# Kernel optimization log

Measured on AMD Instinct MI355X. Metric: run time of the kernel, lower is better.

Reference implementation:

```python
import jax, jax.numpy as jnp
import numpy as np

B, S, I, H = 2, 400, 80, 128
F = 2 * H            # bidirectional feature dim
N = S + 1            # zero row prepended -> pairwise grid size
MAX_SEG = 50
NCLS = 50


def prelu(x, a):
    return jnp.where(x >= 0, x, a * x)


def lstm_dir(x, Wi, Wh, b, reverse=False):
    # x: (B, S, I); torch gate order: i, f, g, o
    if reverse:
        x = x[:, ::-1]
    Hd = Wh.shape[1]

    def step(carry, xt):
        h, c = carry
        gates = xt @ Wi.T + h @ Wh.T + b
        i_, f_, g_, o_ = jnp.split(gates, 4, axis=-1)
        c = jax.nn.sigmoid(f_) * c + jax.nn.sigmoid(i_) * jnp.tanh(g_)
        h = jax.nn.sigmoid(o_) * jnp.tanh(c)
        return (h, c), h

    h0 = jnp.zeros((x.shape[0], Hd), x.dtype)
    _, hs = jax.lax.scan(step, (h0, h0), jnp.swapaxes(x, 0, 1))
    hs = jnp.swapaxes(hs, 0, 1)
    if reverse:
        hs = hs[:, ::-1]
    return hs


def setup_inputs() -> dict:
    key = jax.random.key(0)
    ks = jax.random.split(key, 16)

    def rn(k, shape, s=0.05):
        return jax.random.normal(k, shape, jnp.float32) * s

    inp = {
        "x": jax.random.normal(ks[0], (B, S, I), jnp.float32),
        "lengths": jnp.full((B,), S, jnp.int32),
        "Wi_f": rn(ks[1], (4 * H, I)), "Wh_f": rn(ks[2], (4 * H, H)), "b_f": jnp.zeros((4 * H,), jnp.float32),
        "Wi_b": rn(ks[3], (4 * H, I)), "Wh_b": rn(ks[4], (4 * H, H)), "b_b": jnp.zeros((4 * H,), jnp.float32),
        "a1": jnp.full((1,), 0.25, jnp.float32),
        "W1": rn(ks[5], (100, 3 * F)), "b1": jnp.zeros((100,), jnp.float32),
        "a2": jnp.full((1,), 0.25, jnp.float32),
        "W2": rn(ks[6], (1, 100)), "b2": jnp.zeros((1,), jnp.float32),
        "ac1": jnp.full((1,), 0.25, jnp.float32),
        "Wc1": rn(ks[7], (2 * NCLS, F)), "bc1": jnp.zeros((2 * NCLS,), jnp.float32),
        "ac2": jnp.full((1,), 0.25, jnp.float32),
        "Wc2": rn(ks[8], (NCLS, 2 * NCLS)), "bc2": jnp.zeros((NCLS,), jnp.float32),
        "ab1": jnp.full((1,), 0.25, jnp.float32),
        "Wb1": rn(ks[9], (2 * NCLS, F)), "bb1": jnp.zeros((2 * NCLS,), jnp.float32),
        "ab2": jnp.full((1,), 0.25, jnp.float32),
        "Wb2": rn(ks[10], (2, 2 * NCLS)), "bb2": jnp.zeros((2,), jnp.float32),
    }
    return inp


def compute_scores(x, Wi_f, Wh_f, b_f, Wi_b, Wh_b, b_b, a1, W1, b1, a2, W2, b2):
    rnn_out = jnp.concatenate(
        [lstm_dir(x, Wi_f, Wh_f, b_f, False), lstm_dir(x, Wi_b, Wh_b, b_b, True)], axis=-1
    )  # (B, S, F)
    xp = jnp.concatenate([jnp.zeros((x.shape[0], 1, F), x.dtype), rnn_out], axis=1)  # (B, N, F)
    cum = jnp.cumsum(xp, axis=1)
    # phi[b,i,j] = concat(cum[j]-cum[i], xp[i], xp[j]); PReLU is elementwise with a
    # single shared parameter, and the first Linear is additive across the concat
    # blocks, so we decompose W1 instead of materializing the (B,N,N,3F) tensor.
    W1c, W1d, W1e = W1[:, :F], W1[:, F:2 * F], W1[:, 2 * F:]
    pc = prelu(cum[:, None, :, :] - cum[:, :, None, :], a1)  # (B, N, N, F)
    pxd = prelu(xp, a1) @ W1d.T                              # (B, N, 100)
    pxe = prelu(xp, a1) @ W1e.T                              # (B, N, 100)
    h = jnp.einsum('bijf,kf->bijk', pc, W1c) + pxd[:, :, None, :] + pxe[:, None, :, :] + b1
    scores = (prelu(h, a2) @ W2.T + b2)[..., 0]              # (B, N, N)
    return rnn_out, scores


def segment_search(scores):
    # DP: best[i] = max_{max(0,i-MAX_SEG) <= k < i} best[k] + scores[:, k, i]
    Bn, Nn = scores.shape[0], scores.shape[1]
    ks = jnp.arange(Nn)

    def dp_step(best, i):
        col = jnp.take(scores, i, axis=2)                    # (B, N)
        mask = (ks >= i - MAX_SEG) & (ks < i)
        cand = jnp.where(mask[None, :], best + col, -jnp.inf)
        m = cand.max(axis=1)
        k = cand.argmax(axis=1)
        best = best.at[:, i].set(m)
        return best, k

    best0 = jnp.zeros((Bn, Nn), scores.dtype)
    best, prev_tail = jax.lax.scan(dp_step, best0, jnp.arange(1, Nn))
    prev = jnp.concatenate([jnp.zeros((Bn, 1), jnp.int32),
                            prev_tail.T.astype(jnp.int32)], axis=1)  # (B, N)
    return best, prev


def reference(x, lengths, Wi_f, Wh_f, b_f, Wi_b, Wh_b, b_b, a1, W1, b1, a2, W2, b2,
              ac1, Wc1, bc1, ac2, Wc2, bc2, ab1, Wb1, bb1, ab2, Wb2, bb2):
    rnn_out, scores = compute_scores(x, Wi_f, Wh_f, b_f, Wi_b, Wh_b, b_b,
                                     a1, W1, b1, a2, W2, b2)
    cls_out = prelu(prelu(rnn_out, ac1) @ Wc1.T + bc1, ac2) @ Wc2.T + bc2
    bin_out = prelu(prelu(rnn_out, ab1) @ Wb1.T + bb1, ab2) @ Wb2.T + bb2
    best, prev = segment_search(scores)
    # pred score for the best segmentation ending at `lengths[b]` equals best[b, L]
    pred_scores = best[jnp.arange(scores.shape[0]), lengths]
    return scores, cls_out, bin_out, pred_scores, prev
```

## Files before the change

kernel.cpp:

```cpp
#include <hip/hip_runtime.h>
#include <hip/hip_fp16.h>
#include <math.h>

#define BB 2
#define SS 400
#define II 80
#define HH 128
#define FF 256
#define NN 401
#define G4 512
#define MAXSEG 50
#define NCLS 50
#define KH 100
#define KP 112
#define FRAGF 14336

#define SCORES_OFF 0
#define CLS_OFF    (BB*NN*NN)
#define BIN_OFF    (CLS_OFF + BB*SS*NCLS)
#define PRED_OFF   (BIN_OFF + BB*SS*2)
#define PREV_OFF   (PRED_OFF + BB)

#define WS_GX      0
#define WS_RNN     (WS_GX + 4*SS*G4)
#define WS_CUM     (WS_RNN + BB*SS*FF)
#define WS_PXD     (WS_CUM + BB*NN*FF)
#define WS_PXE     (WS_PXD + BB*NN*KP)
#define WS_PART    (WS_PXE + BB*NN*KP)
#define WS_W2P     (WS_PART + BB*16*FF)
#define WS_B1P     (WS_W2P + KP)
#define WS_WHP     (WS_B1P + KP)
#define WS_WFRAGC  (WS_WHP + 65536)
#define WS_WFRAGD  (WS_WFRAGC + FRAGF)
#define WS_WFRAGE  (WS_WFRAGD + FRAGF)
#define WS_WFRAGHC (WS_WFRAGE + FRAGF)
#define WS_WFRAGHB (WS_WFRAGHC + FRAGF)
#define WS_BC1P    (WS_WFRAGHB + FRAGF)
#define WS_BB1P    (WS_BC1P + KP)

typedef __attribute__((ext_vector_type(8))) short short8;
typedef __attribute__((ext_vector_type(4))) float f32x4;
typedef _Float16 f16x2 __attribute__((ext_vector_type(2)));
typedef _Float16 f16x8 __attribute__((ext_vector_type(8)));

__device__ __forceinline__ float prelu_f(float x, float a) {
    return x >= 0.f ? x : a * x;
}
__device__ __forceinline__ unsigned short f2bf(float x) {
    union { float f; unsigned u; } v; v.f = x;
    unsigned r = v.u + 0x7fffu + ((v.u >> 16) & 1u);
    return (unsigned short)(r >> 16);
}
__device__ __forceinline__ unsigned cvt_pk_bf16(float lo, float hi) {
    unsigned r;
    asm("v_cvt_pk_bf16_f32 %0, %1, %2" : "=v"(r) : "v"(lo), "v"(hi));
    return r;
}
__device__ __forceinline__ float fast_sigmoid(float x) {
    return 1.f / (1.f + __expf(-x));
}
__device__ __forceinline__ float fast_tanh(float x) {
    return 1.f - 2.f / (1.f + __expf(2.f * x));
}
__device__ __forceinline__ void rec_barrier() {
    __builtin_amdgcn_sched_barrier(0);
    asm volatile("s_waitcnt lgkmcnt(0)");
    __builtin_amdgcn_s_barrier();
    __builtin_amdgcn_sched_barrier(0);
}
__device__ __forceinline__ int fragidx(int k, int f) {
    int kt = k >> 4, l15 = k & 15;
    int ks = f >> 5, quad = (f >> 3) & 3, e = f & 7;
    return ((((kt * 8 + ks) * 4 + quad) * 16) + l15) * 8 + e;
}

#define GXTC 8
#define GXBLKS (4 * (SS / GXTC))
#define PREPBLKS (G4 + GXBLKS)
__global__ void k_lstm_pre(const float* __restrict__ x,
                           const float* __restrict__ Wi_f, const float* __restrict__ b_f,
                           const float* __restrict__ Wi_b, const float* __restrict__ b_b,
                           float* __restrict__ gx,
                           const float* __restrict__ Wh_f, const float* __restrict__ Wh_b,
                           __half* __restrict__ whp) {
    int blk0 = blockIdx.x;
    int tid = threadIdx.x;
    if (blk0 < G4) {
        int gq = blk0;
        int gate = gq >> 7;
        int unit = gq & 127;
        int wv = unit >> 4, col = unit & 15;
        int dir = tid >> 7, k = tid & 127;
        int kt = k >> 5, lanehi = (k >> 3) & 3, e = k & 7;
        int lane = lanehi * 16 + col;
        const float* Wh = dir ? Wh_b : Wh_f;
        whp[(size_t)(((((dir * 4 + gate) * 8 + wv) * 4 + kt) * 64) + lane) * 8 + e] =
            (__half)Wh[gq * HH + k];
        return;
    }
    int gxb = blk0 - G4;
    int db = gxb / (SS / GXTC);
    int tc = gxb % (SS / GXTC);
    int b = db & 1, dir = db >> 1;
    const float* Wi = dir ? Wi_b : Wi_f;
    const float* bias = dir ? b_b : b_f;
    int t0 = tc * GXTC;

    __shared__ __align__(16) float xs[GXTC][II];
    for (int idx = tid; idx < GXTC * II; idx += 256) {
        int tt = idx / II, ii = idx - tt * II;
        int xt = dir ? (SS - 1 - (t0 + tt)) : (t0 + tt);
        xs[tt][ii] = x[(b * SS + xt) * II + ii];
    }
    __syncthreads();

    int g1 = tid + 256;
    const float* w0p = Wi + tid * II;
    const float* w1p = Wi + g1 * II;
    float acc0[GXTC], acc1[GXTC];
    {
        float b0v = bias[tid], b1v = bias[g1];
#pragma unroll
        for (int t = 0; t < GXTC; ++t) { acc0[t] = b0v; acc1[t] = b1v; }
    }
    for (int kc = 0; kc < 5; ++kc) {
        float4 wa0 = *(const float4*)(w0p + kc * 16 + 0);
        float4 wa1 = *(const float4*)(w0p + kc * 16 + 4);
        float4 wa2 = *(const float4*)(w0p + kc * 16 + 8);
        float4 wa3 = *(const float4*)(w0p + kc * 16 + 12);
        float4 wb0 = *(const float4*)(w1p + kc * 16 + 0);
        float4 wb1 = *(const float4*)(w1p + kc * 16 + 4);
        float4 wb2 = *(const float4*)(w1p + kc * 16 + 8);
        float4 wb3 = *(const float4*)(w1p + kc * 16 + 12);
#pragma unroll
        for (int t = 0; t < GXTC; ++t) {
            float4 x0 = *(const float4*)(&xs[t][kc * 16 + 0]);
            float4 x1 = *(const float4*)(&xs[t][kc * 16 + 4]);
            float4 x2 = *(const float4*)(&xs[t][kc * 16 + 8]);
            float4 x3 = *(const float4*)(&xs[t][kc * 16 + 12]);
            acc0[t] += wa0.x * x0.x + wa0.y * x0.y + wa0.z * x0.z + wa0.w * x0.w;
            acc0[t] += wa1.x * x1.x + wa1.y * x1.y + wa1.z * x1.z + wa1.w * x1.w;
            acc0[t] += wa2.x * x2.x + wa2.y * x2.y + wa2.z * x2.z + wa2.w * x2.w;
            acc0[t] += wa3.x * x3.x + wa3.y * x3.y + wa3.z * x3.z + wa3.w * x3.w;
            acc1[t] += wb0.x * x0.x + wb0.y * x0.y + wb0.z * x0.z + wb0.w * x0.w;
            acc1[t] += wb1.x * x1.x + wb1.y * x1.y + wb1.z * x1.z + wb1.w * x1.w;
            acc1[t] += wb2.x * x2.x + wb2.y * x2.y + wb2.z * x2.z + wb2.w * x2.w;
            acc1[t] += wb3.x * x3.x + wb3.y * x3.y + wb3.z * x3.z + wb3.w * x3.w;
        }
    }
#pragma unroll
    for (int t = 0; t < GXTC; ++t) {
        gx[((size_t)(db * SS + t0 + t) * HH + (tid & 127)) * 4 + (tid >> 7)] = acc0[t];
        gx[((size_t)(db * SS + t0 + t) * HH + (g1 & 127)) * 4 + (g1 >> 7)] = acc1[t];
    }
}

#define WPACKS (5 * KP)
__global__ __launch_bounds__(256, 1)
void k_lstm_rec(const _Float16* __restrict__ whf, const float* __restrict__ gxr,
                float* __restrict__ rnn_out,
                const float* __restrict__ W1, const float* __restrict__ W2,
                const float* __restrict__ b1,
                const float* __restrict__ Wc1, const float* __restrict__ Wb1,
                const float* __restrict__ bc1, const float* __restrict__ bb1,
                short* __restrict__ wfC, short* __restrict__ wfD,
                short* __restrict__ wfE, short* __restrict__ wfHC,
                short* __restrict__ wfHB,
                float* __restrict__ w2p, float* __restrict__ b1p,
                float* __restrict__ bc1p, float* __restrict__ bb1p) {
    int tid = threadIdx.x;
    if (blockIdx.x >= 4) {
        int blk0 = blockIdx.x - 4;
        int which = blk0 / KP;
        int k = blk0 % KP;
        float w = 0.f;
        short* dst = wfC;
        if (which == 0)      { if (k < KH) w = W1[k * (3 * FF) + tid];          dst = wfC; }
        else if (which == 1) { if (k < KH) w = W1[k * (3 * FF) + FF + tid];     dst = wfD; }
        else if (which == 2) { if (k < KH) w = W1[k * (3 * FF) + 2 * FF + tid]; dst = wfE; }
        else if (which == 3) { if (k < KH) w = Wc1[k * FF + tid];               dst = wfHC; }
        else                 { if (k < KH) w = Wb1[k * FF + tid];               dst = wfHB; }
        dst[fragidx(k, tid)] = (short)f2bf(w);
        if (tid == 0) {
            if (which == 0) {
                w2p[k] = (k < KH) ? W2[k] : 0.f;
                b1p[k] = (k < KH) ? b1[k] : 0.f;
            } else if (which == 3) {
                bc1p[k] = (k < KH) ? bc1[k] : 0.f;
            } else if (which == 4) {
                bb1p[k] = (k < KH) ? bb1[k] : 0.f;
            }
        }
        return;
    }
    int db = blockIdx.x;
    int b = db & 1, dir = db >> 1;
    int wv = tid >> 6;
    int lane = tid & 63;

    f16x8 bfA[4][4], bfB[4][4];
    {
        const f16x8* wp = (const f16x8*)whf;
#pragma unroll
        for (int g = 0; g < 4; ++g)
#pragma unroll
            for (int kt = 0; kt < 4; ++kt) {
                bfA[g][kt] = wp[((((dir * 4 + g) * 8 + (2 * wv)) * 4 + kt) * 64) + lane];
                bfB[g][kt] = wp[((((dir * 4 + g) * 8 + (2 * wv + 1)) * 4 + kt) * 64) + lane];
            }
    }

    __shared__ __align__(16) __half hsf[2][128];
    (&hsf[0][0])[tid] = (__half)0.f;
    __syncthreads();

    bool act = (lane < 32);
    bool grpB = (lane >= 16);
    int unit = (wv << 5) + (lane & 31);
    float c_state = 0.f;

    const float4* gp4 = (const float4*)gxr + (size_t)(db * SS) * HH + unit;
    float4 g0 = make_float4(0,0,0,0), g1 = g0, g2 = g0, g3 = g0;
    if (act) {
        g0 = gp4[0 * HH];
        g1 = gp4[1 * HH];
        g2 = gp4[2 * HH];
        g3 = gp4[3 * HH];
    }
    const float4* gq = gp4 + (size_t)4 * HH;

    float* outp = rnn_out + ((size_t)b * SS + (dir ? (SS - 1) : 0)) * FF
                + dir * HH + unit;
    const int ostep = dir ? -FF : FF;

    const f32x4 z4 = (f32x4){0.f, 0.f, 0.f, 0.f};
    int pb = 0;
    int hib = (lane >> 4) * 8;
    bool aload = (lane & 3) == 0;

    f16x8 a0v = (f16x8)(_Float16)0.f, a1v = a0v, a2v = a0v, a3v = a0v;

#define REC_STEP(G, PF) do {                                                   \
        if (aload) {                                                           \
            a0v = *(const f16x8*)(&hsf[pb][ 0 + hib]);                         \
            a1v = *(const f16x8*)(&hsf[pb][32 + hib]);                         \
            a2v = *(const f16x8*)(&hsf[pb][64 + hib]);                         \
            a3v = *(const f16x8*)(&hsf[pb][96 + hib]);                         \
        }                                                                      \
        f32x4 aA0 = __builtin_amdgcn_mfma_f32_16x16x32_f16(a0v, bfA[0][0], z4, 0, 0, 0); \
        f32x4 aA1 = __builtin_amdgcn_mfma_f32_16x16x32_f16(a0v, bfA[1][0], z4, 0, 0, 0); \
        f32x4 aA2 = __builtin_amdgcn_mfma_f32_16x16x32_f16(a0v, bfA[2][0], z4, 0, 0, 0); \
        f32x4 aA3 = __builtin_amdgcn_mfma_f32_16x16x32_f16(a0v, bfA[3][0], z4, 0, 0, 0); \
        f32x4 aB0 = __builtin_amdgcn_mfma_f32_16x16x32_f16(a0v, bfB[0][0], z4, 0, 0, 0); \
        f32x4 aB1 = __builtin_amdgcn_mfma_f32_16x16x32_f16(a0v, bfB[1][0], z4, 0, 0, 0); \
        f32x4 aB2 = __builtin_amdgcn_mfma_f32_16x16x32_f16(a0v, bfB[2][0], z4, 0, 0, 0); \
        f32x4 aB3 = __builtin_amdgcn_mfma_f32_16x16x32_f16(a0v, bfB[3][0], z4, 0, 0, 0); \
        aA0 = __builtin_amdgcn_mfma_f32_16x16x32_f16(a1v, bfA[0][1], aA0, 0, 0, 0); \
        aA1 = __builtin_amdgcn_mfma_f32_16x16x32_f16(a1v, bfA[1][1], aA1, 0, 0, 0); \
        aA2 = __builtin_amdgcn_mfma_f32_16x16x32_f16(a1v, bfA[2][1], aA2, 0, 0, 0); \
        aA3 = __builtin_amdgcn_mfma_f32_16x16x32_f16(a1v, bfA[3][1], aA3, 0, 0, 0); \
        aB0 = __builtin_amdgcn_mfma_f32_16x16x32_f16(a1v, bfB[0][1], aB0, 0, 0, 0); \
        aB1 = __builtin_amdgcn_mfma_f32_16x16x32_f16(a1v, bfB[1][1], aB1, 0, 0, 0); \
        aB2 = __builtin_amdgcn_mfma_f32_16x16x32_f16(a1v, bfB[2][1], aB2, 0, 0, 0); \
        aB3 = __builtin_amdgcn_mfma_f32_16x16x32_f16(a1v, bfB[3][1], aB3, 0, 0, 0); \
        aA0 = __builtin_amdgcn_mfma_f32_16x16x32_f16(a2v, bfA[0][2], aA0, 0, 0, 0); \
        aA1 = __builtin_amdgcn_mfma_f32_16x16x32_f16(a2v, bfA[1][2], aA1, 0, 0, 0); \
        aA2 = __builtin_amdgcn_mfma_f32_16x16x32_f16(a2v, bfA[2][2], aA2, 0, 0, 0); \
        aA3 = __builtin_amdgcn_mfma_f32_16x16x32_f16(a2v, bfA[3][2], aA3, 0, 0, 0); \
        aB0 = __builtin_amdgcn_mfma_f32_16x16x32_f16(a2v, bfB[0][2], aB0, 0, 0, 0); \
        aB1 = __builtin_amdgcn_mfma_f32_16x16x32_f16(a2v, bfB[1][2], aB1, 0, 0, 0); \
        aB2 = __builtin_amdgcn_mfma_f32_16x16x32_f16(a2v, bfB[2][2], aB2, 0, 0, 0); \
        aB3 = __builtin_amdgcn_mfma_f32_16x16x32_f16(a2v, bfB[3][2], aB3, 0, 0, 0); \
        aA0 = __builtin_amdgcn_mfma_f32_16x16x32_f16(a3v, bfA[0][3], aA0, 0, 0, 0); \
        aA1 = __builtin_amdgcn_mfma_f32_16x16x32_f16(a3v, bfA[1][3], aA1, 0, 0, 0); \
        aA2 = __builtin_amdgcn_mfma_f32_16x16x32_f16(a3v, bfA[2][3], aA2, 0, 0, 0); \
        aA3 = __builtin_amdgcn_mfma_f32_16x16x32_f16(a3v, bfA[3][3], aA3, 0, 0, 0); \
        aB0 = __builtin_amdgcn_mfma_f32_16x16x32_f16(a3v, bfB[0][3], aB0, 0, 0, 0); \
        aB1 = __builtin_amdgcn_mfma_f32_16x16x32_f16(a3v, bfB[1][3], aB1, 0, 0, 0); \
        aB2 = __builtin_amdgcn_mfma_f32_16x16x32_f16(a3v, bfB[2][3], aB2, 0, 0, 0); \
        aB3 = __builtin_amdgcn_mfma_f32_16x16x32_f16(a3v, bfB[3][3], aB3, 0, 0, 0); \
        if (act) {                                                             \
            float gi = (grpB ? aB0[0] : aA0[0]) + G.x;                         \
            float gf = (grpB ? aB1[0] : aA1[0]) + G.y;                         \
            float gg = (grpB ? aB2[0] : aA2[0]) + G.z;                         \
            float go = (grpB ? aB3[0] : aA3[0]) + G.w;                         \
            if (PF) { G = *gq; gq += HH; }         \
            c_state = fast_sigmoid(gf) * c_state + fast_sigmoid(gi) * fast_tanh(gg); \
            float h = fast_sigmoid(go) * fast_tanh(c_state);                   \
            hsf[pb ^ 1][unit] = (__half)h;                                     \
            *outp = h;                                                         \
            outp += ostep;                                                     \
        }                                                                      \
        rec_barrier();                                                         \
        pb ^= 1;                                                               \
    } while (0)

    for (int it = 0; it < 99; ++it) {
        REC_STEP(g0, 1);
        REC_STEP(g1, 1);
        REC_STEP(g2, 1);
        REC_STEP(g3, 1);
    }
    REC_STEP(g0, 0);
    REC_STEP(g1, 0);
    REC_STEP(g2, 0);
    REC_STEP(g3, 0);
#undef REC_STEP
}

#define PXBLKS 26
#define HDBLKS 25
#define AP 272
#define UCP 116
__global__ __launch_bounds__(256, 2)
void k_cum_mlp(const float* __restrict__ rnn, float* __restrict__ cum,
               const float* __restrict__ a1p,
               const float* __restrict__ ac1p, const float* __restrict__ ab1p,
               const short* __restrict__ wfD, const short* __restrict__ wfE,
               const short* __restrict__ wfHC, const short* __restrict__ wfHB,
               const float* __restrict__ bc1p, const float* __restrict__ bb1p,
               const float* __restrict__ ac2p, const float* __restrict__ ab2p,
               const float* __restrict__ Wc2, const float* __restrict__ bc2,
               const float* __restrict__ Wb2, const float* __restrict__ bb2,
               float* __restrict__ pxd, float* __restrict__ pxe,
               float* __restrict__ cls_out, float* __restrict__ bin_out) {
    int tid = threadIdx.x;
    if (blockIdx.x < BB) {
        int b = blockIdx.x;
        int f = tid;
        float run = 0.f;
        cum[(size_t)(b * NN) * FF + f] = 0.f;
        const float* rp = rnn + (size_t)b * SS * FF + f;
        float* cp = cum + ((size_t)b * NN + 1) * FF + f;
#pragma unroll 8
        for (int t = 0; t < SS; ++t) {
            run += rp[(size_t)t * FF];
            cp[(size_t)t * FF] = run;
        }
        return;
    }
    int blk = blockIdx.x - BB;
    bool is_px = (blk < PXBLKS);
    int rowbase = is_px ? blk * 32 : (blk - PXBLKS) * 32;
    int nrows_tot = is_px ? BB * NN : BB * SS;

    __shared__ __align__(16) short dth[2][32][AP];
    __shared__ float ucsh[2][32][UCP];

    {
        int row = tid >> 3;
        int fb = (tid & 7) * 32;
        int rg = rowbase + row;
        float src[32];
        if (is_px) {
            float a1 = a1p[0];
            int b = rg / NN, n = rg % NN;
            bool valid = (rg < nrows_tot) && (n > 0);
            const float* sp = valid ? (rnn + (b * SS + n - 1) * FF + fb) : nullptr;
#pragma unroll
            for (int c4 = 0; c4 < 8; ++c4) {
                float4 v = valid ? *(const float4*)(sp + c4 * 4) : make_float4(0,0,0,0);
                src[c4*4] = v.x; src[c4*4+1] = v.y; src[c4*4+2] = v.z; src[c4*4+3] = v.w;
            }
            union { short8 s; unsigned u4[4]; } h8;
#pragma unroll
            for (int c8 = 0; c8 < 4; ++c8) {
                float d[8];
#pragma unroll
                for (int e = 0; e < 8; ++e) d[e] = prelu_f(src[c8*8+e], a1);
#pragma unroll
                for (int p = 0; p < 4; ++p) h8.u4[p] = cvt_pk_bf16(d[2*p], d[2*p+1]);
                *(short8*)(&dth[0][row][fb + c8 * 8]) = h8.s;
            }
        } else {
            float ac1 = ac1p[0], ab1 = ab1p[0];
            bool valid = (rg < nrows_tot);
            const float* sp = valid ? (rnn + rg * FF + fb) : nullptr;
#pragma unroll
            for (int c4 = 0; c4 < 8; ++c4) {
                float4 v = valid ? *(const float4*)(sp + c4 * 4) : make_float4(0,0,0,0);
                src[c4*4] = v.x; src[c4*4+1] = v.y; src[c4*4+2] = v.z; src[c4*4+3] = v.w;
            }
            union { short8 s; unsigned u4[4]; } hc, hb;
#pragma unroll
            for (int c8 = 0; c8 < 4; ++c8) {
                float dc[8], dbv[8];
#pragma unroll
                for (int e = 0; e < 8; ++e) {
                    dc[e] = prelu_f(src[c8*8+e], ac1);
                    dbv[e] = prelu_f(src[c8*8+e], ab1);
                }
#pragma unroll
                for (int p = 0; p < 4; ++p) {
                    hc.u4[p] = cvt_pk_bf16(dc[2*p], dc[2*p+1]);
                    hb.u4[p] = cvt_pk_bf16(dbv[2*p], dbv[2*p+1]);
                }
                *(short8*)(&dth[0][row][fb + c8 * 8]) = hc.s;
                *(short8*)(&dth[1][row][fb + c8 * 8]) = hb.s;
            }
        }
    }
    __syncthreads();

    int lane = tid & 63;
    int wv = tid >> 6;
    int quad = lane >> 4;
    int l15 = lane & 15;
    int kt0 = wv * 2, kt1 = wv * 2 + 1;
    bool has1 = (kt1 < 7);

    const short8* wp0 = (const short8*)(is_px ? wfD : wfHC);
    const short8* wp1 = (const short8*)(is_px ? wfE : wfHB);

    f32x4 acc[2][2][2];
#pragma unroll
    for (int p = 0; p < 2; ++p)
#pragma unroll
        for (int mt = 0; mt < 2; ++mt)
#pragma unroll
            for (int kk = 0; kk < 2; ++kk) acc[p][mt][kk] = (f32x4){0.f,0.f,0.f,0.f};

#pragma unroll
    for (int ks = 0; ks < 8; ++ks) {
        short8 b00 = wp0[((kt0 * 8 + ks) * 4 + quad) * 16 + l15];
        short8 b01 = has1 ? wp0[((kt1 * 8 + ks) * 4 + quad) * 16 + l15] : b00;
        short8 b10 = wp1[((kt0 * 8 + ks) * 4 + quad) * 16 + l15];
        short8 b11 = has1 ? wp1[((kt1 * 8 + ks) * 4 + quad) * 16 + l15] : b10;
#pragma unroll
        for (int mt = 0; mt < 2; ++mt) {
            short8 a0 = *(const short8*)(&dth[0][mt * 16 + l15][ks * 32 + quad * 8]);
            short8 a1v = is_px ? a0
                       : *(const short8*)(&dth[1][mt * 16 + l15][ks * 32 + quad * 8]);
            acc[0][mt][0] = __builtin_amdgcn_mfma_f32_16x16x32_bf16(a0, b00, acc[0][mt][0], 0, 0, 0);
            acc[1][mt][0] = __builtin_amdgcn_mfma_f32_16x16x32_bf16(a1v, b10, acc[1][mt][0], 0, 0, 0);
            if (has1) {
                acc[0][mt][1] = __builtin_amdgcn_mfma_f32_16x16x32_bf16(a0, b01, acc[0][mt][1], 0, 0, 0);
                acc[1][mt][1] = __builtin_amdgcn_mfma_f32_16x16x32_bf16(a1v, b11, acc[1][mt][1], 0, 0, 0);
            }
        }
    }

    int kout0 = kt0 * 16 + l15;
    int kout1 = has1 ? (kt1 * 16 + l15) : 0;

    if (is_px) {
#pragma unroll
        for (int mt = 0; mt < 2; ++mt) {
#pragma unroll
            for (int r = 0; r < 4; ++r) {
                int m = mt * 16 + quad * 4 + r;
                int rg = rowbase + m;
                if (rg < nrows_tot) {
                    pxd[rg * KP + kout0] = acc[0][mt][0][r];
                    pxe[rg * KP + kout0] = acc[1][mt][0][r];
                    if (has1) {
                        pxd[rg * KP + kout1] = acc[0][mt][1][r];
                        pxe[rg * KP + kout1] = acc[1][mt][1][r];
                    }
                }
            }
        }
        return;
    }

    float bc0 = bc1p[kout0], bc1v = bc1p[kout1];
    float bb0 = bb1p[kout0], bb1v = bb1p[kout1];
    float ac2 = ac2p[0], ab2 = ab2p[0];
#pragma unroll
    for (int mt = 0; mt < 2; ++mt) {
#pragma unroll
        for (int r = 0; r < 4; ++r) {
            int m = mt * 16 + quad * 4 + r;
            ucsh[0][m][kout0] = prelu_f(acc[0][mt][0][r] + bc0, ac2);
            ucsh[1][m][kout0] = prelu_f(acc[1][mt][0][r] + bb0, ab2);
            if (has1) {
                ucsh[0][m][kout1] = prelu_f(acc[0][mt][1][r] + bc1v, ac2);
                ucsh[1][m][kout1] = prelu_f(acc[1][mt][1][r] + bb1v, ab2);
            }
        }
    }
    __syncthreads();
    {
        int row = tid >> 3;
        int oc = tid & 7;
        int rg = rowbase + row;
        bool valid = (rg < nrows_tot);
        for (int o = oc; o < NCLS; o += 8) {
            float s = bc2[o];
            const float* w = Wc2 + o * KH;
#pragma unroll 4
            for (int k = 0; k < KH; ++k) s += w[k] * ucsh[0][row][k];
            if (valid) cls_out[rg * NCLS + o] = s;
        }
        if (tid < 64) {
            int row2 = tid >> 1, o = tid & 1;
            int rg2 = rowbase + row2;
            float s = bb2[o];
            const float* w = Wb2 + o * KH;
#pragma unroll 4
            for (int k = 0; k < KH; ++k) s += w[k] * ucsh[1][row2][k];
            if (rg2 < nrows_tot) bin_out[rg2 * 2 + o] = s;
        }
    }
}

#define JT 32
#define JTILES 13
#define NP2 201
#define APS 280
#define CIP 264
__global__ __launch_bounds__(256, 3)
void k_scores(const float* __restrict__ cum,
              const short* __restrict__ wfrag,
              const float* __restrict__ pxd, const float* __restrict__ pxe,
              const float* __restrict__ b1p, const float* __restrict__ w2p,
              const float* __restrict__ b2p,
              const float* __restrict__ a1p, const float* __restrict__ a2p,
              float* __restrict__ scores, float* __restrict__ dpcol) {
    int blk = blockIdx.x;
    int jt = blk % JTILES;
    int ipair = (blk / JTILES) % NP2;
    int b = blk / (JTILES * NP2);
    int tid = threadIdx.x;
    float a1 = a1p[0], a2 = a2p[0];
    int jbase = jt * JT;
    int i0 = ipair * 2;
    int i1 = i0 + 1;
    bool has_i1 = (i1 <= SS);
    int i1c = has_i1 ? i1 : i0;

    __shared__ __align__(16) float cish[2][CIP];
    __shared__ __align__(16) short dth[2][JT][APS];
    __shared__ float red[2][4][JT];

    cish[0][tid + (tid >> 5)] = cum[(b * NN + i0) * FF + tid];
    cish[1][tid + (tid >> 5)] = cum[(b * NN + i1c) * FF + tid];
    __syncthreads();

    {
        int row = tid >> 3;
        int fb = (tid & 7) * 32;
        int fbq = fb + (tid & 7);
        int jg = jbase + row;
        int jc = (jg <= SS) ? jg : SS;
        const float* cj = cum + (b * NN + jc) * FF + fb;
        float4 v[8];
#pragma unroll
        for (int c8 = 0; c8 < 4; ++c8) {
            v[2 * c8] = *(const float4*)(cj + c8 * 8);
            v[2 * c8 + 1] = *(const float4*)(cj + c8 * 8 + 4);
        }
#pragma unroll
        for (int ii = 0; ii < 2; ++ii) {
            const float* cio = &cish[ii][0];
#pragma unroll
            for (int c8 = 0; c8 < 4; ++c8) {
                float dv[8] = { v[2*c8].x, v[2*c8].y, v[2*c8].z, v[2*c8].w,
                                v[2*c8+1].x, v[2*c8+1].y, v[2*c8+1].z, v[2*c8+1].w };
                float d[8];
#pragma unroll
                for (int e = 0; e < 8; ++e)
                    d[e] = prelu_f(dv[e] - cio[fbq + c8 * 8 + e], a1);
                union { short8 s; unsigned u4[4]; } h8;
#pragma unroll
                for (int p = 0; p < 4; ++p) h8.u4[p] = cvt_pk_bf16(d[2*p], d[2*p+1]);
                *(short8*)(&dth[ii][row][fb + c8 * 8]) = h8.s;
            }
        }
    }
    __syncthreads();

    int lane = tid & 63;
    int wv = tid >> 6;
    int quad = lane >> 4;
    int l15 = lane & 15;
    int kt0 = wv * 2, kt1 = wv * 2 + 1;
    bool has1 = (kt1 < 7);

    const short8* wf = (const short8*)wfrag;
    f32x4 acc[2][2][2];
#pragma unroll
    for (int ii = 0; ii < 2; ++ii)
#pragma unroll
        for (int mt = 0; mt < 2; ++mt)
#pragma unroll
            for (int kk = 0; kk < 2; ++kk) acc[ii][mt][kk] = (f32x4){0.f,0.f,0.f,0.f};

#pragma unroll
    for (int ks = 0; ks < 8; ++ks) {
        short8 b0 = wf[((kt0 * 8 + ks) * 4 + quad) * 16 + l15];
        short8 b1v = has1 ? wf[((kt1 * 8 + ks) * 4 + quad) * 16 + l15] : b0;
#pragma unroll
        for (int ii = 0; ii < 2; ++ii) {
#pragma unroll
            for (int mt = 0; mt < 2; ++mt) {
                short8 a = *(const short8*)(&dth[ii][mt * 16 + l15][ks * 32 + quad * 8]);
                acc[ii][mt][0] = __builtin_amdgcn_mfma_f32_16x16x32_bf16(a, b0, acc[ii][mt][0], 0, 0, 0);
                if (has1)
                    acc[ii][mt][1] = __builtin_amdgcn_mfma_f32_16x16x32_bf16(a, b1v, acc[ii][mt][1], 0, 0, 0);
            }
        }
    }

    int kout0 = kt0 * 16 + l15;
    int kout1 = has1 ? (kt1 * 16 + l15) : 0;
    float bb0 = b1p[kout0], bb1v = b1p[kout1];
    float w20 = w2p[kout0];
    float w21 = has1 ? w2p[kout1] : 0.f;

#pragma unroll
    for (int ii = 0; ii < 2; ++ii) {
        int iv = ii ? i1c : i0;
        float pd0 = pxd[(b * NN + iv) * KP + kout0];
        float pd1 = pxd[(b * NN + iv) * KP + kout1];
#pragma unroll
        for (int mt = 0; mt < 2; ++mt) {
#pragma unroll
            for (int r = 0; r < 4; ++r) {
                int m = mt * 16 + quad * 4 + r;
                int jg = jbase + m;
                int jc = (jg <= SS) ? jg : SS;
                float pe0 = pxe[(b * NN + jc) * KP + kout0];
                float pe1 = pxe[(b * NN + jc) * KP + kout1];
                float h0 = acc[ii][mt][0][r] + pd0 + pe0 + bb0;
                float s = w20 * prelu_f(h0, a2);
                float h1 = acc[ii][mt][1][r] + pd1 + pe1 + bb1v;
                s += w21 * prelu_f(h1, a2);
                s += __shfl_xor(s, 1);
                s += __shfl_xor(s, 2);
                s += __shfl_xor(s, 4);
                s += __shfl_xor(s, 8);
                if (l15 == 0) red[ii][wv][m] = s;
            }
        }
    }
    __syncthreads();
    if (tid < 2 * JT) {
        int ii = tid >> 5;
        int jl = tid & 31;
        int jg = jbase + jl;
        int iv = ii ? i1 : i0;
        if (jg <= SS && (ii == 0 || has_i1)) {
            float tot = red[ii][0][jl] + red[ii][1][jl] + red[ii][2][jl] + red[ii][3][jl] + b2p[0];
            scores[(b * NN + iv) * NN + jg] = tot;
            int d = jg - iv;
            if (d >= 1 && d <= MAXSEG) {
                dpcol[(b * NN + jg) * 64 + (iv & 63)] = tot;
            }
        }
    }
}

__global__ void k_dp(const float* __restrict__ dpcol, const int* __restrict__ lengths,
                     float* __restrict__ predF, float* __restrict__ prevF) {
    int b = blockIdx.x;
    int lane = threadIdx.x;
    int len = lengths[b];
    if (lane == 0) prevF[b * NN] = 0.f;

    float blr = 0.f;
    float predv = 0.f;

#define LO(I) (((I) > MAXSEG) ? ((I) - MAXSEG) : 0)
#define LOADCOL(ii) \
    ( ((ii) <= SS && (((lane - LO(ii)) & 63) < ((ii) - LO(ii)))) \
        ? dpcol[(b * NN + (ii)) * 64 + lane] : 0.f )

    float u0 = LOADCOL(1),  u1 = LOADCOL(2),  u2 = LOADCOL(3),  u3 = LOADCOL(4);
    float u4 = LOADCOL(5),  u5 = LOADCOL(6),  u6 = LOADCOL(7),  u7 = LOADCOL(8);
    float u8 = LOADCOL(9),  u9 = LOADCOL(10), u10 = LOADCOL(11), u11 = LOADCOL(12);
    float u12 = LOADCOL(13), u13 = LOADCOL(14), u14 = LOADCOL(15), u15 = LOADCOL(16);

#define DPP_MAX2(CTRL, va, vb) do {                                           \
        int _ta = __builtin_amdgcn_update_dpp(__float_as_int(va),             \
                      __float_as_int(va), (CTRL), 0xF, 0xF, false);           \
        int _tb = __builtin_amdgcn_update_dpp(__float_as_int(vb),             \
                      __float_as_int(vb), (CTRL), 0xF, 0xF, false);           \
        (va) = fmaxf((va), __int_as_float(_ta));                              \
        (vb) = fmaxf((vb), __int_as_float(_tb));                              \
    } while (0)

#define DP_STEP2(I, BUFA, BUFB) do {                                          \
        int loA_ = LO(I);                                                     \
        int cntA_ = (I) - loA_;                                               \
        int loB_ = LO((I) + 1);                                               \
        int cntBm_ = (I) - loB_;                   \
        int offA_ = (lane - loA_) & 63;                                       \
        int offB_ = (lane - loB_) & 63;                                       \
        float vA0_ = (offA_ < cntA_) ? blr + BUFA : -INFINITY;                \
        float vB0_ = (offB_ < cntBm_) ? blr + BUFB : -INFINITY;               \
        float vA_ = vA0_, vB_ = vB0_;                                         \
        DPP_MAX2(0x111, vA_, vB_);                            \
        DPP_MAX2(0x112, vA_, vB_);                            \
        DPP_MAX2(0x114, vA_, vB_);                            \
        DPP_MAX2(0x118, vA_, vB_);                            \
        DPP_MAX2(0x142, vA_, vB_);                          \
        DPP_MAX2(0x143, vA_, vB_);                          \
        float mA_ = __int_as_float(                                           \
            __builtin_amdgcn_readlane(__float_as_int(vA_), 63));              \
        float mB_ = __int_as_float(                                           \
            __builtin_amdgcn_readlane(__float_as_int(vB_), 63));              \
        float sI_ = __int_as_float(                                           \
            __builtin_amdgcn_readlane(__float_as_int(BUFB), (I) & 63));       \
        float candI_ = mA_ + sI_;                                             \
        bool takeI_ = candI_ > mB_;                                           \
        float mBf_ = takeI_ ? candI_ : mB_;                                   \
        unsigned long long mkA_ = __ballot(vA0_ == mA_);                      \
        unsigned long long mkB_ = __ballot(vB0_ == mB_);                      \
        int rotA_ = loA_ & 63;                                                \
        int rotB_ = loB_ & 63;                                                \
        unsigned long long mrA_ = rotA_ ? ((mkA_ >> rotA_) | (mkA_ << (64 - rotA_))) : mkA_; \
        unsigned long long mrB_ = rotB_ ? ((mkB_ >> rotB_) | (mkB_ << (64 - rotB_))) : mkB_; \
        int kbA_ = loA_ + (__ffsll(mrA_) - 1);                                \
        int kbB_ = takeI_ ? (I) : (loB_ + (__ffsll(mrB_) - 1));               \
        if (lane == 0) {                                                      \
            prevF[b * NN + (I)] = (float)kbA_;                                \
            prevF[b * NN + (I) + 1] = (float)kbB_;                            \
            if ((I) == len) predv = mA_;                                      \
            if ((I) + 1 == len) predv = mBf_;                                 \
        }                                                                     \
        if (lane == ((I) & 63)) blr = mA_;                                    \
        if (lane == (((I) + 1) & 63)) blr = mBf_;                             \
    } while (0)

    for (int i = 1; i <= SS; i += 16) {
        DP_STEP2(i,      u0,  u1);  u0 = LOADCOL(i + 16);  u1 = LOADCOL(i + 17);
        DP_STEP2(i + 2,  u2,  u3);  u2 = LOADCOL(i + 18);  u3 = LOADCOL(i + 19);
        DP_STEP2(i + 4,  u4,  u5);  u4 = LOADCOL(i + 20);  u5 = LOADCOL(i + 21);
        DP_STEP2(i + 6,  u6,  u7);  u6 = LOADCOL(i + 22);  u7 = LOADCOL(i + 23);
        DP_STEP2(i + 8,  u8,  u9);  u8 = LOADCOL(i + 24);  u9 = LOADCOL(i + 25);
        DP_STEP2(i + 10, u10, u11); u10 = LOADCOL(i + 26); u11 = LOADCOL(i + 27);
        DP_STEP2(i + 12, u12, u13); u12 = LOADCOL(i + 28); u13 = LOADCOL(i + 29);
        DP_STEP2(i + 14, u14, u15); u14 = LOADCOL(i + 30); u15 = LOADCOL(i + 31);
    }
#undef DP_STEP2
#undef DPP_MAX2
#undef LOADCOL
#undef LO
    if (lane == 0) predF[b] = predv;
}

extern "C" void kernel_launch(void* const* d_in, const int* in_sizes, int n_in,
                              void* d_out, int out_size, void* d_ws, size_t ws_size,
                              hipStream_t stream) {
    const float* x    = (const float*)d_in[0];
    const int* lengths= (const int*)d_in[1];
    const float* Wi_f = (const float*)d_in[2];
    const float* Wh_f = (const float*)d_in[3];
    const float* b_f  = (const float*)d_in[4];
    const float* Wi_b = (const float*)d_in[5];
    const float* Wh_b = (const float*)d_in[6];
    const float* b_b  = (const float*)d_in[7];
    const float* a1   = (const float*)d_in[8];
    const float* W1   = (const float*)d_in[9];
    const float* b1   = (const float*)d_in[10];
    const float* a2   = (const float*)d_in[11];
    const float* W2   = (const float*)d_in[12];
    const float* b2   = (const float*)d_in[13];
    const float* ac1  = (const float*)d_in[14];
    const float* Wc1  = (const float*)d_in[15];
    const float* bc1  = (const float*)d_in[16];
    const float* ac2  = (const float*)d_in[17];
    const float* Wc2  = (const float*)d_in[18];
    const float* bc2  = (const float*)d_in[19];
    const float* ab1  = (const float*)d_in[20];
    const float* Wb1  = (const float*)d_in[21];
    const float* bb1  = (const float*)d_in[22];
    const float* ab2  = (const float*)d_in[23];
    const float* Wb2  = (const float*)d_in[24];
    const float* bb2  = (const float*)d_in[25];

    float* out = (float*)d_out;
    float* scores = out + SCORES_OFF;
    float* cls    = out + CLS_OFF;
    float* bin    = out + BIN_OFF;
    float* pred   = out + PRED_OFF;
    float* prev   = out + PREV_OFF;

    float* ws    = (float*)d_ws;
    float* gx    = ws + WS_GX;
    float* dpcol = ws + WS_GX;
    float* rnn   = ws + WS_RNN;
    float* cum   = ws + WS_CUM;
    float* pxd   = ws + WS_PXD;
    float* pxe   = ws + WS_PXE;
    float* w2p   = ws + WS_W2P;
    float* b1p   = ws + WS_B1P;
    __half* whp  = (__half*)(ws + WS_WHP);
    short* wfC   = (short*)(ws + WS_WFRAGC);
    short* wfD   = (short*)(ws + WS_WFRAGD);
    short* wfE   = (short*)(ws + WS_WFRAGE);
    short* wfHC  = (short*)(ws + WS_WFRAGHC);
    short* wfHB  = (short*)(ws + WS_WFRAGHB);
    float* bc1p  = ws + WS_BC1P;
    float* bb1p  = ws + WS_BB1P;

    k_lstm_pre<<<PREPBLKS, 256, 0, stream>>>(x, Wi_f, b_f, Wi_b, b_b, gx,
                                             Wh_f, Wh_b, whp);
    k_lstm_rec<<<4 + WPACKS, 256, 0, stream>>>((const _Float16*)whp, gx, rnn,
                                               W1, W2, b1, Wc1, Wb1, bc1, bb1,
                                               wfC, wfD, wfE, wfHC, wfHB,
                                               w2p, b1p, bc1p, bb1p);
    k_cum_mlp<<<BB + PXBLKS + HDBLKS, 256, 0, stream>>>(rnn, cum, a1, ac1, ab1,
                                                        wfD, wfE, wfHC, wfHB,
                                                        bc1p, bb1p, ac2, ab2,
                                                        Wc2, bc2, Wb2, bb2,
                                                        pxd, pxe, cls, bin);
    k_scores<<<BB * NP2 * JTILES, 256, 0, stream>>>(cum, wfC, pxd, pxe, b1p, w2p, b2,
                                                    a1, a2, scores, dpcol);
    k_dp<<<BB, 64, 0, stream>>>(dpcol, lengths, pred, prev);
}
```

Baseline: 524.1 us.

## Merge both LSTM directions into one 512-thread block per batch

The recurrent LSTM kernel now runs both directions of a batch element in one 512-thread block, with 4 waves per direction and separate shared hidden-state buffers, instead of one 256-thread block per (batch, direction). The aim is to let waves from both directions share a CU's SIMDs and interleave their MFMA and activation work to hide per-step latency. In exchange, each step's barrier now waits on 8 waves across two independent recurrences, which couples their timing. The weight-packing blocks are also launched at 512 threads, with the upper half returning immediately.

New measurement: 624.6 us. 1.19x slower.

```diff
diff --git a/kernel.cpp b/kernel.cpp
--- a/kernel.cpp
+++ b/kernel.cpp
@@ -156,7 +156,7 @@
 }
 
 #define WPACKS (5 * KP)
-__global__ __launch_bounds__(256, 1)
+__global__ __launch_bounds__(512, 1)
 void k_lstm_rec(const _Float16* __restrict__ whf, const float* __restrict__ gxr,
                 float* __restrict__ rnn_out,
                 const float* __restrict__ W1, const float* __restrict__ W2,
@@ -169,8 +169,9 @@
                 float* __restrict__ w2p, float* __restrict__ b1p,
                 float* __restrict__ bc1p, float* __restrict__ bb1p) {
     int tid = threadIdx.x;
-    if (blockIdx.x >= 4) {
-        int blk0 = blockIdx.x - 4;
+    if (blockIdx.x >= BB) {
+        if (tid >= 256) return;
+        int blk0 = blockIdx.x - BB;
         int which = blk0 / KP;
         int k = blk0 % KP;
         float w = 0.f;
@@ -193,10 +194,12 @@
         }
         return;
     }
-    int db = blockIdx.x;
-    int b = db & 1, dir = db >> 1;
+    int b = blockIdx.x;
     int wv = tid >> 6;
+    int dir = wv >> 2;
+    int wvd = wv & 3;
     int lane = tid & 63;
+    int db = dir * 2 + b;
 
     f16x8 bfA[4][4], bfB[4][4];
     {
@@ -205,18 +208,18 @@
         for (int g = 0; g < 4; ++g)
 #pragma unroll
             for (int kt = 0; kt < 4; ++kt) {
-                bfA[g][kt] = wp[((((dir * 4 + g) * 8 + (2 * wv)) * 4 + kt) * 64) + lane];
-                bfB[g][kt] = wp[((((dir * 4 + g) * 8 + (2 * wv + 1)) * 4 + kt) * 64) + lane];
-            }
-    }
-
-    __shared__ __align__(16) __half hsf[2][128];
-    (&hsf[0][0])[tid] = (__half)0.f;
+                bfA[g][kt] = wp[((((dir * 4 + g) * 8 + (2 * wvd)) * 4 + kt) * 64) + lane];
+                bfB[g][kt] = wp[((((dir * 4 + g) * 8 + (2 * wvd + 1)) * 4 + kt) * 64) + lane];
+            }
+    }
+
+    __shared__ __align__(16) __half hsf[2][2][128];
+    (&hsf[0][0][0])[tid] = (__half)0.f;
     __syncthreads();
 
     bool act = (lane < 32);
     bool grpB = (lane >= 16);
-    int unit = (wv << 5) + (lane & 31);
+    int unit = (wvd << 5) + (lane & 31);
     float c_state = 0.f;
 
     const float4* gp4 = (const float4*)gxr + (size_t)(db * SS) * HH + unit;
@@ -242,10 +245,10 @@
 
 #define REC_STEP(G, PF) do {                                                   \
         if (aload) {                                                           \
-            a0v = *(const f16x8*)(&hsf[pb][ 0 + hib]);                         \
-            a1v = *(const f16x8*)(&hsf[pb][32 + hib]);                         \
-            a2v = *(const f16x8*)(&hsf[pb][64 + hib]);                         \
-            a3v = *(const f16x8*)(&hsf[pb][96 + hib]);                         \
+            a0v = *(const f16x8*)(&hsf[dir][pb][ 0 + hib]);                    \
+            a1v = *(const f16x8*)(&hsf[dir][pb][32 + hib]);                    \
+            a2v = *(const f16x8*)(&hsf[dir][pb][64 + hib]);                    \
+            a3v = *(const f16x8*)(&hsf[dir][pb][96 + hib]);                    \
         }                                                                      \
         f32x4 aA0 = __builtin_amdgcn_mfma_f32_16x16x32_f16(a0v, bfA[0][0], z4, 0, 0, 0); \
         f32x4 aA1 = __builtin_amdgcn_mfma_f32_16x16x32_f16(a0v, bfA[1][0], z4, 0, 0, 0); \
@@ -287,7 +290,7 @@
             if (PF) { G = *gq; gq += HH; }         \
             c_state = fast_sigmoid(gf) * c_state + fast_sigmoid(gi) * fast_tanh(gg); \
             float h = fast_sigmoid(go) * fast_tanh(c_state);                   \
-            hsf[pb ^ 1][unit] = (__half)h;                                     \
+            hsf[dir][pb ^ 1][unit] = (__half)h;                                \
             *outp = h;                                                         \
             outp += ostep;                                                     \
         }                                                                      \
@@ -797,10 +800,10 @@
 
     k_lstm_pre<<<PREPBLKS, 256, 0, stream>>>(x, Wi_f, b_f, Wi_b, b_b, gx,
                                              Wh_f, Wh_b, whp);
-    k_lstm_rec<<<4 + WPACKS, 256, 0, stream>>>((const _Float16*)whp, gx, rnn,
-                                               W1, W2, b1, Wc1, Wb1, bc1, bb1,
-                                               wfC, wfD, wfE, wfHC, wfHB,
-                                               w2p, b1p, bc1p, bb1p);
+    k_lstm_rec<<<BB + WPACKS, 512, 0, stream>>>((const _Float16*)whp, gx, rnn,
+                                                W1, W2, b1, Wc1, Wb1, bc1, bb1,
+                                                wfC, wfD, wfE, wfHC, wfHB,
+                                                w2p, b1p, bc1p, bb1p);
     k_cum_mlp<<<BB + PXBLKS + HDBLKS, 256, 0, stream>>>(rnn, cum, a1, ac1, ab1,
                                                         wfD, wfE, wfHC, wfHB,
                                                         bc1p, bb1p, ac2, ab2,
```
